# Kernel tuning notes

Measured on AMD Instinct MI355X. Metric: run time of the kernel, lower is better.

## Reference

```python
import jax, jax.numpy as jnp
import numpy as np

B, D, E, K = 8192, 1024, 8, 5  # batch, in_dim, num_size_classes, num_depth_classes
H = max(64, D)                 # hidden = max(64, in_dim)
EPS = 1e-8


def ordinal_logits_to_probs(logits, num_classes):
    # logits: [B, K-1] cumulative ordinal logits -> [B, K] class probs
    q = jax.nn.sigmoid(logits)
    probs = jnp.concatenate(
        [1.0 - q[:, :1], q[:, :-1] - q[:, 1:], q[:, -1:]], axis=1
    )  # [B, K]
    probs = jnp.clip(probs, EPS)
    return probs / jnp.clip(probs.sum(axis=1, keepdims=True), EPS)


def setup_inputs() -> dict:
    key = jax.random.key(0)
    kx, ks, k1, k2 = jax.random.split(key, 4)
    x = jax.random.normal(kx, (B, D), dtype=jnp.float32)
    size_idx = jax.random.randint(ks, (B,), 0, E, dtype=jnp.int64)
    # per-expert 2-layer MLP params: Linear(D,H) -> ReLU -> Linear(H,K-1)
    W1 = jax.random.normal(k1, (E, D, H), dtype=jnp.float32) / np.sqrt(D)
    b1 = jnp.zeros((E, H), dtype=jnp.float32)
    W2 = jax.random.normal(k2, (E, H, K - 1), dtype=jnp.float32) / np.sqrt(H)
    b2 = jnp.zeros((E, K - 1), dtype=jnp.float32)
    return {"x": x, "size_idx": size_idx, "W1": W1, "b1": b1, "W2": W2, "b2": b2}


def reference(x, size_idx, W1, b1, W2, b2):
    # Hard routing: each token gets the output of expert size_idx[b].
    # Dense all-expert compute + per-token select (same math as mask/gather/scatter,
    # dropout is inference-mode identity).
    h = jax.nn.relu(jnp.einsum('bd,edh->beh', x, W1) + b1)      # [B, E, H]
    all_logits = jnp.einsum('beh,ehk->bek', h, W2) + b2          # [B, E, K-1]
    idx = size_idx.astype(jnp.int32)[:, None, None]              # [B, 1, 1]
    logits = jnp.take_along_axis(all_logits, idx, axis=1)[:, 0]  # [B, K-1]
    probs = ordinal_logits_to_probs(logits, K)                   # [B, K]
    return logits, probs
```

## Files before the change

### kernel.cpp

```cpp
#include <hip/hip_runtime.h>
#include <cstdint>
#include <cstddef>

#define Bn 8192
#define Dn 1024
#define Hn 1024
#define En 8
#define MT 128
#define MTILES (PERM_N / MT)
#define PERM_N (Bn + En * MT)
#define NB 16

#define NXB 4096
#define NWB 2048
#define XB0 1
#define WB0 (XB0 + NXB)
#define TOTB (WB0 + NWB)

typedef unsigned short u16;
typedef __bf16 bf16x8 __attribute__((ext_vector_type(8)));
typedef float f32x4 __attribute__((ext_vector_type(4)));
typedef unsigned short ushort8 __attribute__((ext_vector_type(8)));

__device__ __forceinline__ u16 f2bf(float f) {
  unsigned int u = __float_as_uint(f);
  unsigned int r = u + 0x7fffu + ((u >> 16) & 1u);
  return (u16)(r >> 16);
}

__device__ __forceinline__ void gld16(const void* g, void* l) {
  __builtin_amdgcn_global_load_lds(
      (const __attribute__((address_space(1))) void*)g,
      (__attribute__((address_space(3))) void*)l, 16, 0, 0);
}

#define PIPE_BARRIER_VM3() do {                    \
    asm volatile("" ::: "memory");                 \
    __builtin_amdgcn_s_waitcnt(0x0F73);            \
    __builtin_amdgcn_s_barrier();                  \
    asm volatile("" ::: "memory");                 \
  } while (0)
#define PIPE_BARRIER_VM0() do {                    \
    asm volatile("" ::: "memory");                 \
    __builtin_amdgcn_s_waitcnt(0x0F70);            \
    __builtin_amdgcn_s_barrier();                  \
    asm volatile("" ::: "memory");                 \
  } while (0)

__global__ __launch_bounds__(256) void prep_k(
    const float* __restrict__ x, const int* __restrict__ sidx,
    const float* __restrict__ W1,
    u16* __restrict__ xb, u16* __restrict__ w1t,
    int* __restrict__ off, int* __restrict__ perm) {
  int bid = blockIdx.x;
  int t = threadIdx.x;

  if (bid == 0) {
    __shared__ int hist[4][En];
    __shared__ int base[4][En];
    __shared__ int eoff[En + 1];
    int wv = t >> 6;
    if (t < 4 * En) ((int*)hist)[t] = 0;
#pragma unroll
    for (int i = 0; i < PERM_N / 256; i++) perm[t + i * 256] = -1;
    __syncthreads();
    int e32[32], r32[32];
#pragma unroll
    for (int i = 0; i < 32; i++) {
      int e = sidx[t + i * 256];
      e32[i] = e;
      r32[i] = atomicAdd(&hist[wv][e], 1);
    }
    __syncthreads();
    if (t < En) {
      int s = 0;
      for (int w = 0; w < 4; w++) { base[w][t] = s; s += hist[w][t]; }
      hist[0][t] = s;
    }
    __syncthreads();
    if (t == 0) {
      int o = 0;
      for (int e = 0; e < En; e++) {
        eoff[e] = o; off[e] = o;
        o += (hist[0][e] + MT - 1) & ~(MT - 1);
      }
      eoff[En] = o; off[En] = o;
    }
    __syncthreads();
#pragma unroll
    for (int i = 0; i < 32; i++) {
      int e = e32[i];
      perm[eoff[e] + base[wv][e] + r32[i]] = t + i * 256;
    }
  } else if (bid < WB0) {
    size_t idx = ((size_t)(bid - XB0) * 256 + t) * 8;
    const float* src = x + idx;
    float4 a = *(const float4*)src;
    float4 b = *(const float4*)(src + 4);
    ushort8 o;
    o[0] = f2bf(a.x); o[1] = f2bf(a.y); o[2] = f2bf(a.z); o[3] = f2bf(a.w);
    o[4] = f2bf(b.x); o[5] = f2bf(b.y); o[6] = f2bf(b.z); o[7] = f2bf(b.w);
    *(ushort8*)(xb + idx) = o;
  } else {
    __shared__ float tile[64][65];
    int wb = bid - WB0;
    int e = wb >> 8;
    int k0 = ((wb >> 4) & 15) * 64;
    int n0 = (wb & 15) * 64;
    int c4 = (t & 15) * 4;
    int r0 = t >> 4;
    const float* src = W1 + ((size_t)e << 20) + (size_t)k0 * Hn + n0;
#pragma unroll
    for (int i = 0; i < 4; i++) {
      int r = r0 + i * 16;
      float4 v = *(const float4*)(src + (size_t)r * Hn + c4);
      tile[r][c4 + 0] = v.x; tile[r][c4 + 1] = v.y;
      tile[r][c4 + 2] = v.z; tile[r][c4 + 3] = v.w;
    }
    __syncthreads();
    u16* dst = w1t + ((size_t)e << 20) + (size_t)n0 * Dn + k0;
#pragma unroll
    for (int i = 0; i < 4; i++) {
      int h = r0 + i * 16;
      ushort4 o;
      o.x = f2bf(tile[c4 + 0][h]);
      o.y = f2bf(tile[c4 + 1][h]);
      o.z = f2bf(tile[c4 + 2][h]);
      o.w = f2bf(tile[c4 + 3][h]);
      *(ushort4*)(dst + (size_t)h * Dn + c4) = o;
    }
  }
}

__global__ __launch_bounds__(256) void gemm_k(
    const u16* __restrict__ xb, const u16* __restrict__ w1t,
    const float* __restrict__ b1, const float* __restrict__ w2,
    const int* __restrict__ off, const int* __restrict__ perm,
    float* __restrict__ partials) {
  __shared__ u16 As[3][4096];
  __shared__ u16 Bs[3][2048];

  int n0 = blockIdx.x * 64;
  int row0 = blockIdx.y * MT;
  if (row0 >= off[En]) return;
  int e = 0;
  while (row0 >= off[e + 1]) e++;

  int tid = threadIdx.x;
  int lane = tid & 63, w = tid >> 6;

  int srow = lane >> 2;
  int slot = lane & 3;
  int scol = (slot ^ ((srow >> 1) & 3)) * 8;
  const u16* aG[2];
  int lOffA[2];
#pragma unroll
  for (int j = 0; j < 2; j++) {
    int rl = 32 * w + 16 * j + srow;
    int tok = perm[row0 + rl];
    if (tok < 0) tok = 0;
    aG[j] = xb + ((size_t)tok << 10) + scol;
    lOffA[j] = (32 * w + 16 * j) * 32;
  }
  const u16* bG = w1t + ((size_t)e << 20) + (size_t)(n0 + 16 * w + srow) * Dn + scol;
  int lOffB = (16 * w) * 32;

  f32x4 acc[2][4];
#pragma unroll
  for (int i = 0; i < 2; i++)
#pragma unroll
    for (int j = 0; j < 4; j++)
      acc[i][j] = (f32x4){0.f, 0.f, 0.f, 0.f};

  int fr = lane & 15;
  int qf = lane >> 4;
  int qs = (qf ^ ((fr >> 1) & 3)) * 8;
  int offA[2], offB[4];
#pragma unroll
  for (int i = 0; i < 2; i++)
    offA[i] = (w * 32 + i * 16 + fr) * 32 + qs;
#pragma unroll
  for (int j = 0; j < 4; j++)
    offB[j] = (j * 16 + fr) * 32 + qs;

#pragma unroll
  for (int it = 0; it < 2; it++) {
    int ko = it * 32;
    gld16(aG[0] + ko, (u16*)As[it] + lOffA[0]);
    gld16(aG[1] + ko, (u16*)As[it] + lOffA[1]);
    gld16(bG + ko, (u16*)Bs[it] + lOffB);
  }

#pragma unroll
  for (int i = 0; i < 31; i++) {
    PIPE_BARRIER_VM3();
    if (i + 2 < 32) {
      int s = (i + 2) % 3;
      int ko = (i + 2) * 32;
      gld16(aG[0] + ko, (u16*)As[s] + lOffA[0]);
      gld16(aG[1] + ko, (u16*)As[s] + lOffA[1]);
      gld16(bG + ko, (u16*)Bs[s] + lOffB);
    }
    const u16* Ab = (const u16*)As[i % 3];
    const u16* Bb = (const u16*)Bs[i % 3];
    bf16x8 af[2], bfr[4];
#pragma unroll
    for (int ii = 0; ii < 2; ii++) af[ii] = *(const bf16x8*)(Ab + offA[ii]);
#pragma unroll
    for (int jj = 0; jj < 4; jj++) bfr[jj] = *(const bf16x8*)(Bb + offB[jj]);
#pragma unroll
    for (int ii = 0; ii < 2; ii++)
#pragma unroll
      for (int jj = 0; jj < 4; jj++)
        acc[ii][jj] = __builtin_amdgcn_mfma_f32_16x16x32_bf16(af[ii], bfr[jj], acc[ii][jj], 0, 0, 0);
  }
  {
    PIPE_BARRIER_VM0();
    const u16* Ab = (const u16*)As[31 % 3];
    const u16* Bb = (const u16*)Bs[31 % 3];
    bf16x8 af[2], bfr[4];
#pragma unroll
    for (int ii = 0; ii < 2; ii++) af[ii] = *(const bf16x8*)(Ab + offA[ii]);
#pragma unroll
    for (int jj = 0; jj < 4; jj++) bfr[jj] = *(const bf16x8*)(Bb + offB[jj]);
#pragma unroll
    for (int ii = 0; ii < 2; ii++)
#pragma unroll
      for (int jj = 0; jj < 4; jj++)
        acc[ii][jj] = __builtin_amdgcn_mfma_f32_16x16x32_bf16(af[ii], bfr[jj], acc[ii][jj], 0, 0, 0);
  }

  float4 w2v[4]; float b1v[4];
#pragma unroll
  for (int j = 0; j < 4; j++) {
    int col = n0 + j * 16 + fr;
    w2v[j] = *(const float4*)(w2 + ((size_t)e * Hn + col) * 4);
    b1v[j] = b1[(size_t)e * Hn + col];
  }
  int chunk = blockIdx.x;
#pragma unroll
  for (int i = 0; i < 2; i++) {
    int rbase = w * 32 + i * 16 + qf * 4;
#pragma unroll
    for (int r = 0; r < 4; r++) {
      float s0 = 0.f, s1 = 0.f, s2 = 0.f, s3 = 0.f;
#pragma unroll
      for (int j = 0; j < 4; j++) {
        float h = acc[i][j][r] + b1v[j];
        h = fmaxf(h, 0.f);
        s0 = fmaf(h, w2v[j].x, s0);
        s1 = fmaf(h, w2v[j].y, s1);
        s2 = fmaf(h, w2v[j].z, s2);
        s3 = fmaf(h, w2v[j].w, s3);
      }
#pragma unroll
      for (int m = 1; m < 16; m <<= 1) {
        s0 += __shfl_xor(s0, m);
        s1 += __shfl_xor(s1, m);
        s2 += __shfl_xor(s2, m);
        s3 += __shfl_xor(s3, m);
      }
      if (fr == 0) {
        int row = row0 + rbase + r;
        *(float4*)(partials + ((size_t)row * NB + chunk) * 4) =
            make_float4(s0, s1, s2, s3);
      }
    }
  }
}

__global__ void probs_k(const float* __restrict__ partials,
                        const int* __restrict__ perm, const int* __restrict__ off,
                        const int* __restrict__ sidx, const float* __restrict__ b2,
                        float* __restrict__ out) {
  int p = blockIdx.x * blockDim.x + threadIdx.x;
  if (p >= off[En]) return;
  int tok = perm[p];
  if (tok < 0) return;
  int e = sidx[tok];
  float s0 = 0.f, s1 = 0.f, s2 = 0.f, s3 = 0.f;
#pragma unroll
  for (int nb = 0; nb < NB; nb++) {
    float4 v = *(const float4*)(partials + ((size_t)p * NB + nb) * 4);
    s0 += v.x; s1 += v.y; s2 += v.z; s3 += v.w;
  }
  float l0 = s0 + b2[e * 4 + 0];
  float l1 = s1 + b2[e * 4 + 1];
  float l2 = s2 + b2[e * 4 + 2];
  float l3 = s3 + b2[e * 4 + 3];
  out[tok * 4 + 0] = l0; out[tok * 4 + 1] = l1;
  out[tok * 4 + 2] = l2; out[tok * 4 + 3] = l3;
  float q0 = 1.f / (1.f + expf(-l0));
  float q1 = 1.f / (1.f + expf(-l1));
  float q2 = 1.f / (1.f + expf(-l2));
  float q3 = 1.f / (1.f + expf(-l3));
  const float eps = 1e-8f;
  float p0 = fmaxf(1.f - q0, eps);
  float p1 = fmaxf(q0 - q1, eps);
  float p2 = fmaxf(q1 - q2, eps);
  float p3 = fmaxf(q2 - q3, eps);
  float p4 = fmaxf(q3, eps);
  float s = p0 + p1 + p2 + p3 + p4;
  float inv = 1.f / fmaxf(s, eps);
  float* pr = out + (size_t)Bn * 4 + (size_t)tok * 5;
  pr[0] = p0 * inv; pr[1] = p1 * inv; pr[2] = p2 * inv;
  pr[3] = p3 * inv; pr[4] = p4 * inv;
}

extern "C" void kernel_launch(void* const* d_in, const int* in_sizes, int n_in,
                              void* d_out, int out_size, void* d_ws, size_t ws_size,
                              hipStream_t stream) {
  const float* x  = (const float*)d_in[0];
  const int* sidx = (const int*)d_in[1];
  const float* W1 = (const float*)d_in[2];
  const float* b1 = (const float*)d_in[3];
  const float* W2 = (const float*)d_in[4];
  const float* b2 = (const float*)d_in[5];
  float* out = (float*)d_out;

  uint8_t* w = (uint8_t*)d_ws;
  int* off  = (int*)(w + 64);
  int* perm = (int*)(w + 512);
  u16* xb      = (u16*)(w + 40960);
  u16* w1t     = (u16*)(w + 40960 + 16777216);
  float* parts = (float*)(w + 40960 + 2 * 16777216);

  prep_k<<<TOTB, 256, 0, stream>>>(x, sidx, W1, xb, w1t, off, perm);
  gemm_k<<<dim3(16, MTILES), 256, 0, stream>>>(xb, w1t, b1, W2, off, perm, parts);
  probs_k<<<(PERM_N + 255) / 256, 256, 0, stream>>>(parts, perm, off, sidx, b2, out);
}
```

Baseline: 164.3 us.

## Enlarge GEMM block tile to 128x128 with 8 waves in a 4x2 grid

The grouped GEMM block now covers 128 rows by 128 hidden columns using 512 threads arranged as 4x2 waves, where before it covered 64 columns with 256 threads. Each thread issues one A load and one B load per k-step, so the waitcnt threshold drops from 3 to 2 outstanding loads. The aim is to halve how many times the gathered activation rows are reloaded across column blocks and to raise arithmetic intensity per block. In exchange, LDS use per block grows and the grid has half as many blocks, which may lower occupancy and leave some CUs idle.

New measurement: 157.0 us. -4.5%, faster.

```diff
diff --git a/kernel.cpp b/kernel.cpp
--- a/kernel.cpp
+++ b/kernel.cpp
@@ -34,9 +34,9 @@
       (__attribute__((address_space(3))) void*)l, 16, 0, 0);
 }
 
-#define PIPE_BARRIER_VM3() do {                    \
+#define PIPE_BARRIER_VM2() do {                    \
     asm volatile("" ::: "memory");                 \
-    __builtin_amdgcn_s_waitcnt(0x0F73);            \
+    __builtin_amdgcn_s_waitcnt(0x0F72);            \
     __builtin_amdgcn_s_barrier();                  \
     asm volatile("" ::: "memory");                 \
   } while (0)
@@ -132,15 +132,15 @@
   }
 }
 
-__global__ __launch_bounds__(256) void gemm_k(
+__global__ __launch_bounds__(512) void gemm_k(
     const u16* __restrict__ xb, const u16* __restrict__ w1t,
     const float* __restrict__ b1, const float* __restrict__ w2,
     const int* __restrict__ off, const int* __restrict__ perm,
     float* __restrict__ partials) {
   __shared__ u16 As[3][4096];
-  __shared__ u16 Bs[3][2048];
-
-  int n0 = blockIdx.x * 64;
+  __shared__ u16 Bs[3][4096];
+
+  int n0 = blockIdx.x * 128;
   int row0 = blockIdx.y * MT;
   if (row0 >= off[En]) return;
   int e = 0;
@@ -148,22 +148,17 @@
 
   int tid = threadIdx.x;
   int lane = tid & 63, w = tid >> 6;
+  int wm = w >> 1, wn = w & 1;
 
   int srow = lane >> 2;
   int slot = lane & 3;
   int scol = (slot ^ ((srow >> 1) & 3)) * 8;
-  const u16* aG[2];
-  int lOffA[2];
-#pragma unroll
-  for (int j = 0; j < 2; j++) {
-    int rl = 32 * w + 16 * j + srow;
-    int tok = perm[row0 + rl];
-    if (tok < 0) tok = 0;
-    aG[j] = xb + ((size_t)tok << 10) + scol;
-    lOffA[j] = (32 * w + 16 * j) * 32;
-  }
-  const u16* bG = w1t + ((size_t)e << 20) + (size_t)(n0 + 16 * w + srow) * Dn + scol;
-  int lOffB = (16 * w) * 32;
+  int rl = 16 * w + srow;
+  int tokA = perm[row0 + rl];
+  if (tokA < 0) tokA = 0;
+  const u16* aG = xb + ((size_t)tokA << 10) + scol;
+  const u16* bG = w1t + ((size_t)e << 20) + (size_t)(n0 + rl) * Dn + scol;
+  int lOff = (16 * w) * 32;
 
   f32x4 acc[2][4];
 #pragma unroll
@@ -178,28 +173,26 @@
   int offA[2], offB[4];
 #pragma unroll
   for (int i = 0; i < 2; i++)
-    offA[i] = (w * 32 + i * 16 + fr) * 32 + qs;
+    offA[i] = (wm * 32 + i * 16 + fr) * 32 + qs;
 #pragma unroll
   for (int j = 0; j < 4; j++)
-    offB[j] = (j * 16 + fr) * 32 + qs;
+    offB[j] = (wn * 64 + j * 16 + fr) * 32 + qs;
 
 #pragma unroll
   for (int it = 0; it < 2; it++) {
     int ko = it * 32;
-    gld16(aG[0] + ko, (u16*)As[it] + lOffA[0]);
-    gld16(aG[1] + ko, (u16*)As[it] + lOffA[1]);
-    gld16(bG + ko, (u16*)Bs[it] + lOffB);
+    gld16(aG + ko, (u16*)As[it] + lOff);
+    gld16(bG + ko, (u16*)Bs[it] + lOff);
   }
 
 #pragma unroll
   for (int i = 0; i < 31; i++) {
-    PIPE_BARRIER_VM3();
+    PIPE_BARRIER_VM2();
     if (i + 2 < 32) {
       int s = (i + 2) % 3;
       int ko = (i + 2) * 32;
-      gld16(aG[0] + ko, (u16*)As[s] + lOffA[0]);
-      gld16(aG[1] + ko, (u16*)As[s] + lOffA[1]);
-      gld16(bG + ko, (u16*)Bs[s] + lOffB);
+      gld16(aG + ko, (u16*)As[s] + lOff);
+      gld16(bG + ko, (u16*)Bs[s] + lOff);
     }
     const u16* Ab = (const u16*)As[i % 3];
     const u16* Bb = (const u16*)Bs[i % 3];
@@ -233,14 +226,14 @@
   float4 w2v[4]; float b1v[4];
 #pragma unroll
   for (int j = 0; j < 4; j++) {
-    int col = n0 + j * 16 + fr;
+    int col = n0 + wn * 64 + j * 16 + fr;
     w2v[j] = *(const float4*)(w2 + ((size_t)e * Hn + col) * 4);
     b1v[j] = b1[(size_t)e * Hn + col];
   }
-  int chunk = blockIdx.x;
+  int chunk = blockIdx.x * 2 + wn;
 #pragma unroll
   for (int i = 0; i < 2; i++) {
-    int rbase = w * 32 + i * 16 + qf * 4;
+    int rbase = wm * 32 + i * 16 + qf * 4;
 #pragma unroll
     for (int r = 0; r < 4; r++) {
       float s0 = 0.f, s1 = 0.f, s2 = 0.f, s3 = 0.f;
@@ -326,6 +319,6 @@
   float* parts = (float*)(w + 40960 + 2 * 16777216);
 
   prep_k<<<TOTB, 256, 0, stream>>>(x, sidx, W1, xb, w1t, off, perm);
-  gemm_k<<<dim3(16, MTILES), 256, 0, stream>>>(xb, w1t, b1, W2, off, perm, parts);
+  gemm_k<<<dim3(8, MTILES), 512, 0, stream>>>(xb, w1t, b1, W2, off, perm, parts);
   probs_k<<<(PERM_N + 255) / 256, 256, 0, stream>>>(parts, perm, off, sidx, b2, out);
 }
```
